# Kernel optimization log

Measured on AMD Instinct MI355X. Metric: run time of the kernel, lower is better.

Reference implementation:

```python
import jax, jax.numpy as jnp
import numpy as np

N, S, H, FA = 16, 64, 256, 256  # batch, sentences, memory_size, fact_attn_hidden


def setup_inputs() -> dict:
    key = jax.random.key(0)
    ks = jax.random.split(key, 12)
    g = lambda k, shp: (jax.random.normal(k, shp, jnp.float32) * 0.05)
    return dict(
        facts=jax.random.normal(ks[0], (N, S, H), jnp.float32),
        prevM=jax.random.normal(ks[1], (N, S, H), jnp.float32),
        questions=jax.random.normal(ks[2], (N, S, H), jnp.float32),
        doc_len=jax.random.randint(ks[3], (N,), S // 2, S + 1),
        z1_w=g(ks[4], (FA, 4 * H)), z1_b=jnp.zeros((FA,), jnp.float32),
        z2_w=g(ks[5], (1, FA)), z2_b=jnp.zeros((1,), jnp.float32),
        Wr_w=g(ks[6], (H, H)), Wr_b=jnp.zeros((H,), jnp.float32),
        Ur_w=g(ks[7], (H, H)), Ur_b=jnp.zeros((H,), jnp.float32),
        W_w=g(ks[8], (H, H)), W_b=jnp.zeros((H,), jnp.float32),
        U_w=g(ks[9], (H, H)), U_b=jnp.zeros((H,), jnp.float32),
        nm_w=g(ks[10], (H, 3 * H)), nm_b=jnp.zeros((H,), jnp.float32),
    )


def reference(facts, prevM, questions, doc_len,
              z1_w, z1_b, z2_w, z2_b,
              Wr_w, Wr_b, Ur_w, Ur_b, W_w, W_b, U_w, U_b,
              nm_w, nm_b):
    n, s, h = facts.shape
    # ---- make_interaction: pairwise features (query axis = dim1, fact/key axis = dim2)
    f = facts[:, None, :, :]       # (N,1,S,H) broadcast over queries
    m = prevM[:, :, None, :]       # (N,S,1,H) broadcast over keys
    q = questions[:, :, None, :]   # (N,S,1,H)
    z = jnp.concatenate([f * q, f * m, jnp.abs(f - q), jnp.abs(f - m)], axis=-1)  # (N,S,S,4H)
    Gh = jnp.tanh(z @ z1_w.T + z1_b)               # (N,S,S,FA)
    G = (Gh @ z2_w.T + z2_b)[..., 0]               # (N,S,S)
    mask = (jnp.arange(s) < doc_len[:, None]).astype(G.dtype)  # (N,S) key mask
    Gm = G * mask[:, None, :]
    Gm = jnp.where(Gm == 0, -jnp.inf, Gm)          # faithful to G[G==0] = -inf
    attn = jax.nn.softmax(Gm, axis=2)              # (N,S,S)

    # ---- AttentionalGRU over the S facts for each of the N*S query rows
    B = n * s
    fb = jnp.broadcast_to(facts[:, None], (n, s, s, h)).reshape(B, s, h)  # (B,S,H)
    gb = attn.reshape(B, s)                                               # (B,S)

    def step(C, xs):
        fact, gt = xs                                   # fact: (B,H), gt: (B,)
        r = jax.nn.sigmoid(fact @ Wr_w.T + Wr_b + C @ Ur_w.T + Ur_b)
        h_t = jnp.tanh(fact @ W_w.T + W_b + r * (C @ U_w.T + U_b))
        gt = gt[:, None]
        return gt * h_t + (1.0 - gt) * C, None

    C0 = jnp.zeros((B, h), facts.dtype)
    C, _ = jax.lax.scan(step, C0, (fb.transpose(1, 0, 2), gb.T))  # scan over S steps
    C = C.reshape(n, s, h)

    # ---- memory update (dropouts are identity in eval mode)
    concat = jnp.concatenate([prevM, C, questions], axis=-1)  # (N,S,3H)
    next_mem = jax.nn.relu(concat @ nm_w.T + nm_b)            # (N,S,H)
    return next_mem, attn
```

## Files before the change

### kernel.cpp

```cpp
#include <hip/hip_runtime.h>
#include <hip/hip_bf16.h>
#include <math.h>

#define NB 16
#define SS 64
#define HH 256
#define FAA 256

using short8 = __attribute__((ext_vector_type(8))) short;
using f32x4  = __attribute__((ext_vector_type(4))) float;

__device__ __forceinline__ unsigned int cvtpk(float a, float b) {
  unsigned int r;
  asm("v_cvt_pk_bf16_f32 %0, %1, %2" : "=v"(r) : "v"(a), "v"(b));
  return r;
}
__device__ __forceinline__ float sel4(const f32x4 a, int q) {
  const float s01 = (q & 1) ? a[1] : a[0];
  const float s23 = (q & 1) ? a[3] : a[2];
  return (q & 2) ? s23 : s01;
}

__global__ __launch_bounds__(256) void prolog_fused(
    const float* __restrict__ z1w, const float* __restrict__ Ur,
    const float* __restrict__ U, const float* __restrict__ nmw,
    const float* __restrict__ pm, const float* __restrict__ qs,
    unsigned short* __restrict__ z1wbf, unsigned short* __restrict__ wcatbf,
    unsigned short* __restrict__ nmbf, unsigned short* __restrict__ pmbf,
    unsigned short* __restrict__ qbf,
    const float* __restrict__ facts, const float* __restrict__ Wr,
    const float* __restrict__ Wrb, const float* __restrict__ Urb,
    const float* __restrict__ Ww, const float* __restrict__ Wb,
    float* __restrict__ FWr, float* __restrict__ FW) {
  __shared__ float fl[4][HH];
  const int bid = blockIdx.x, tid = threadIdx.x;

  auto cvt8 = [&](const float* src, unsigned short* dst, int base) {
    const float4 a = *(const float4*)(src + base);
    const float4 b = *(const float4*)(src + base + 4);
    uint4 o;
    o.x = cvtpk(a.x, a.y); o.y = cvtpk(a.z, a.w);
    o.z = cvtpk(b.x, b.y); o.w = cvtpk(b.z, b.w);
    *(uint4*)(dst + base) = o;
  };
  auto cvt8perm = [&](const float* row, unsigned short* dst, int sbase, int c0) {
    const float4 lo = *(const float4*)(row + c0);
    const float4 hi = *(const float4*)(row + c0 + 16);
    uint4 o;
    o.x = cvtpk(lo.x, hi.x); o.y = cvtpk(lo.y, hi.y);
    o.z = cvtpk(lo.z, hi.z); o.w = cvtpk(lo.w, hi.w);
    *(uint4*)(dst + sbase) = o;
  };

  if (bid < 128) {
    const int base = (bid * 256 + tid) * 8;
    cvt8(z1w, z1wbf, base);
    return;
  }
  if (bid < 192) {
    const int base = ((bid - 128) * 256 + tid) * 8;
    const int o = base >> 8, s0 = base & 255;
    const int gb = s0 & ~31, t0 = s0 & 31;
    const float* row = (o < 256) ? (Ur + o * 256) : (U + (o - 256) * 256);
    cvt8perm(row, wcatbf, base, gb + (t0 >> 1));
    return;
  }
  if (bid < 288) {
    const int base = ((bid - 192) * 256 + tid) * 8;
    const int o = base / 768, k0 = base - o * 768;
    const float* row = nmw + o * 768;
    if (k0 >= 256 && k0 < 512) {
      const int s0 = k0 - 256, gb = s0 & ~31, t0 = s0 & 31;
      cvt8perm(row, nmbf, base, 256 + gb + (t0 >> 1));
    } else {
      cvt8(row, nmbf + o * 768, k0);
    }
    return;
  }
  if (bid < 416) {
    const int base = ((bid - 288) * 256 + tid) * 8;
    cvt8(pm, pmbf, base);
    return;
  }
  if (bid < 544) {
    const int base = ((bid - 416) * 256 + tid) * 8;
    cvt8(qs, qbf, base);
    return;
  }
  const int b0 = (bid - 544) * 4;
#pragma unroll
  for (int r = 0; r < 4; ++r) fl[r][tid] = facts[(b0 + r) * HH + tid];
  __syncthreads();
  float ar[4] = {0.f, 0.f, 0.f, 0.f}, aw[4] = {0.f, 0.f, 0.f, 0.f};
  const float4* wr = (const float4*)(Wr + tid * HH);
  const float4* ww = (const float4*)(Ww + tid * HH);
  for (int d4 = 0; d4 < 64; ++d4) {
    float4 a = wr[d4], b = ww[d4];
#pragma unroll
    for (int r = 0; r < 4; ++r) {
      float4 f = *(const float4*)&fl[r][d4 * 4];
      ar[r] += a.x * f.x + a.y * f.y + a.z * f.z + a.w * f.w;
      aw[r] += b.x * f.x + b.y * f.y + b.z * f.z + b.w * f.w;
    }
  }
  const float br = Wrb[tid] + Urb[tid], bw = Wb[tid];
#pragma unroll
  for (int r = 0; r < 4; ++r) {
    FWr[(b0 + r) * HH + tid] = ar[r] + br;
    FW[(b0 + r) * HH + tid] = aw[r] + bw;
  }
}

__global__ __launch_bounds__(512, 4) void gate_gemm(
    const float* __restrict__ facts, const float* __restrict__ prevM,
    const float* __restrict__ questions, const unsigned short* __restrict__ z1wbf,
    const float* __restrict__ z1b, const float* __restrict__ z2w,
    const float* __restrict__ z2b, const int* __restrict__ doc_len,
    float* __restrict__ attn) {
  __shared__ unsigned short Ab[3][128 * 32];
  __shared__ unsigned short Bb[3][256 * 32];
  __shared__ float Gpart[128][4];

  const int bi = blockIdx.x;
  const int n = bi >> 5, i0 = (bi & 31) * 2;
  const int tid = threadIdx.x;
  const int w = tid >> 6, l = tid & 63;
  const int rg = w >> 2, cg = w & 3;
  const int l15 = l & 15, q = l >> 4;
  const int t15 = tid & 15, jb = tid >> 4;

  const float* fn = facts + n * SS * HH;
  const float* qn = questions + (n * SS + i0) * HH;
  const float* mn = prevM + (n * SS + i0) * HH;

  auto stageB = [&](int buf, int c) {
    const int kb = (c & 3) * 256 + (c >> 2) * 32;
    const int swz = ((l & 3) ^ ((l >> 2) & 3)) * 8;
#pragma unroll
    for (int j = 0; j < 2; ++j) {
      const int colg = w * 32 + j * 16 + (l >> 2);
      const unsigned short* src = z1wbf + colg * 1024 + kb + swz;
      __builtin_amdgcn_global_load_lds(src, Bb[buf] + (w * 32 + j * 16) * 32, 16, 0, 0);
    }
  };

  auto buildA = [&](int buf, int s, float2 f0, float2 f1, float2 q0, float2 q1,
                    float2 m0, float2 m1) {
    unsigned int* dst = (unsigned int*)Ab[buf];
    const int dsw = t15 ^ ((jb & 3) << 2);
    const float2 o0 = (s & 1) ? m0 : q0;
    const float2 o1 = (s & 1) ? m1 : q1;
#pragma unroll
    for (int pl = 0; pl < 2; ++pl) {
      const float fx = pl ? f1.x : f0.x;
      const float fy = pl ? f1.y : f0.y;
#pragma unroll
      for (int il = 0; il < 2; ++il) {
        const int row = il * 64 + pl * 32 + jb;
        const float ox = il ? o1.x : o0.x;
        const float oy = il ? o1.y : o0.y;
        float a, b;
        if (s < 2) { a = fx * ox;         b = fy * oy; }
        else       { a = fabsf(fx - ox);  b = fabsf(fy - oy); }
        dst[row * 16 + dsw] = cvtpk(a, b);
      }
    }
  };

  const f32x4 zero4 = {0.f, 0.f, 0.f, 0.f};
  f32x4 acc[4][4];
#pragma unroll
  for (int a = 0; a < 4; ++a)
#pragma unroll
    for (int b = 0; b < 4; ++b) acc[a][b] = zero4;

  auto mfmaStep = [&](int buf) {
    short8 Bfr[4];
#pragma unroll
    for (int nf = 0; nf < 4; ++nf) {
      const int col = cg * 64 + nf * 16 + l15;
      Bfr[nf] = *(const short8*)&Bb[buf][col * 32 + (q ^ (l15 & 3)) * 8];
    }
    __builtin_amdgcn_s_setprio(1);
#pragma unroll
    for (int mf = 0; mf < 4; ++mf) {
      const int row = rg * 64 + mf * 16 + l15;
      const short8 Afm = *(const short8*)&Ab[buf][row * 32 + (q ^ (l15 & 3)) * 8];
#pragma unroll
      for (int nf = 0; nf < 4; ++nf)
        acc[mf][nf] = __builtin_amdgcn_mfma_f32_16x16x32_bf16(Afm, Bfr[nf], acc[mf][nf], 0, 0, 0);
    }
    __builtin_amdgcn_s_setprio(0);
  };

  const int hh2 = t15 * 2;
  auto pf = [&](int hc, float2& f0, float2& f1, float2& q0, float2& q1,
                float2& m0, float2& m1) {
    const int h = hc * 32 + hh2;
    f0 = *(const float2*)(fn + jb * HH + h);
    f1 = *(const float2*)(fn + (jb + 32) * HH + h);
    q0 = *(const float2*)(qn + h);
    q1 = *(const float2*)(qn + HH + h);
    m0 = *(const float2*)(mn + h);
    m1 = *(const float2*)(mn + HH + h);
  };

  float2 Rf0, Rf1, Rq0, Rq1, Rm0, Rm1;
  float2 Sf0, Sf1, Sq0, Sq1, Sm0, Sm1;
  pf(0, Rf0, Rf1, Rq0, Rq1, Rm0, Rm1);
  stageB(0, 0);
  stageB(1, 1);
  buildA(0, 0, Rf0, Rf1, Rq0, Rq1, Rm0, Rm1);
  asm volatile("s_waitcnt vmcnt(2) lgkmcnt(0)\n\ts_barrier" ::: "memory");

#pragma unroll
  for (int c = 0; c < 32; ++c) {
    const int s = c & 3, hc = c >> 2;
    const int cb = c % 3, nb2 = (c + 1) % 3, fb = (c + 2) % 3;
    const bool pfphase = (s == 2) && (hc < 7);

    if (c + 2 < 32) stageB(fb, c + 2);
    if (pfphase) pf(hc + 1, Sf0, Sf1, Sq0, Sq1, Sm0, Sm1);
    if (c + 1 < 32) {
      if (((c + 1) & 3) == 0)
        buildA(nb2, 0, Sf0, Sf1, Sq0, Sq1, Sm0, Sm1);
      else
        buildA(nb2, (c + 1) & 3, Rf0, Rf1, Rq0, Rq1, Rm0, Rm1);
    }
    mfmaStep(cb);

    if (c <= 29) {
      if (pfphase)
        asm volatile("s_waitcnt vmcnt(8) lgkmcnt(0)\n\ts_barrier" ::: "memory");
      else
        asm volatile("s_waitcnt vmcnt(2) lgkmcnt(0)\n\ts_barrier" ::: "memory");
    } else if (c == 30) {
      asm volatile("s_waitcnt vmcnt(0) lgkmcnt(0)\n\ts_barrier" ::: "memory");
    }
    if (s == 3) {
      Rf0 = Sf0; Rf1 = Sf1; Rq0 = Sq0; Rq1 = Sq1; Rm0 = Sm0; Rm1 = Sm1;
    }
  }

  float psum[4][4];
#pragma unroll
  for (int mf = 0; mf < 4; ++mf)
#pragma unroll
    for (int v = 0; v < 4; ++v) psum[mf][v] = 0.f;

#pragma unroll
  for (int nf = 0; nf < 4; ++nf) {
    const int k = cg * 64 + nf * 16 + l15;
    const float zb = z1b[k], zw = z2w[k];
#pragma unroll
    for (int mf = 0; mf < 4; ++mf)
#pragma unroll
      for (int v = 0; v < 4; ++v) {
        const float x = acc[mf][nf][v] + zb;
        const float e = __expf(2.f * x);
        const float t = 1.f - 2.f / (e + 1.f);
        psum[mf][v] += zw * t;
      }
  }
#pragma unroll
  for (int d = 1; d < 16; d <<= 1)
#pragma unroll
    for (int mf = 0; mf < 4; ++mf)
#pragma unroll
      for (int v = 0; v < 4; ++v) psum[mf][v] += __shfl_xor(psum[mf][v], d, 64);
  if (l15 == 0) {
#pragma unroll
    for (int mf = 0; mf < 4; ++mf)
#pragma unroll
      for (int v = 0; v < 4; ++v)
        Gpart[rg * 64 + mf * 16 + q * 4 + v][cg] = psum[mf][v];
  }
  __syncthreads();
  if (tid < 128) {
    const float gg = Gpart[tid][0] + Gpart[tid][1] + Gpart[tid][2] + Gpart[tid][3] + z2b[0];
    const int i = i0 + (tid >> 6), j = tid & 63;
    const int dl = doc_len[n];
    const float x = (j < dl && gg != 0.0f) ? gg : -INFINITY;
    float mx = x;
#pragma unroll
    for (int d = 1; d < 64; d <<= 1) mx = fmaxf(mx, __shfl_xor(mx, d, 64));
    const float e = (x == -INFINITY) ? 0.f : __expf(x - mx);
    float s = e;
#pragma unroll
    for (int d = 1; d < 64; d <<= 1) s += __shfl_xor(s, d, 64);
    attn[(n * SS + i) * SS + j] = e / s;
  }
}

__global__ __launch_bounds__(512, 2) void gru_scan(
    const unsigned short* __restrict__ wcat, const float* __restrict__ FWr,
    const float* __restrict__ FW, const float* __restrict__ Ub,
    const float* __restrict__ attn, unsigned short* __restrict__ Cout,
    float* __restrict__ cm0save, float* __restrict__ cm1save, const int part) {
  __shared__ unsigned short Cbf[2][4 * 272];
  __shared__ float attn_sT[64 * 4];

  const int bi = blockIdx.x, n = bi >> 4, i0 = (bi & 15) * 4;
  const int tid = threadIdx.x, w = tid >> 6, l = tid & 63;
  const int l15 = l & 15, q = l >> 4;
  const int h0 = w * 32 + l15;

  short8 Bf[8][4];
#pragma unroll
  for (int f = 0; f < 4; ++f) {
    const int wrow = ((f >> 1) ? 256 : 0) + w * 32 + (f & 1) * 16 + l15;
    const unsigned short* bb = wcat + wrow * 256 + q * 8;
#pragma unroll
    for (int kt = 0; kt < 8; ++kt)
      Bf[kt][f] = *(const short8*)(bb + kt * 32);
  }

  const float ub0 = Ub[h0], ub1 = Ub[h0 + 16];

  for (int e = tid; e < 64 * 4; e += 512)
    attn_sT[e] = attn[(n * SS + i0 + (e & 3)) * SS + (e >> 2)];

  float cm0, cm1;
  if (part == 0) {
    for (int e = tid; e < 544; e += 512)
      ((unsigned int*)Cbf[0])[e] = 0u;
    cm0 = 0.f; cm1 = 0.f;
  } else {
    cm0 = cm0save[bi * 512 + tid];
    cm1 = cm1save[bi * 512 + tid];
    ((unsigned int*)Cbf[0])[q * 136 + w * 16 + l15] = cvtpk(cm0, cm1);
  }
  __syncthreads();

  const float* fwr_g = FWr + n * SS * HH;
  const float* fw_g  = FW + n * SS * HH;

  const int tbeg = part ? 32 : 0, tend = part ? 64 : 32;
  float fr0 = fwr_g[tbeg * HH + h0], fr1 = fwr_g[tbeg * HH + h0 + 16];
  float fc0 = fw_g[tbeg * HH + h0],  fc1 = fw_g[tbeg * HH + h0 + 16];

  for (int t = tbeg; t < tend; ++t) {
    const int cur = t & 1;
    const unsigned short* Cr = Cbf[cur];
    unsigned int* Cw = (unsigned int*)Cbf[cur ^ 1];

    short8 Af[8];
    const int arow = (l15 & 3) * 272;
#pragma unroll
    for (int kt = 0; kt < 8; ++kt)
      Af[kt] = *(const short8*)&Cr[arow + kt * 32 + q * 8];

    float nr0 = 0.f, nr1 = 0.f, nc0 = 0.f, nc1 = 0.f;
    if (t < 63) {
      nr0 = fwr_g[(t + 1) * HH + h0];
      nr1 = fwr_g[(t + 1) * HH + h0 + 16];
      nc0 = fw_g[(t + 1) * HH + h0];
      nc1 = fw_g[(t + 1) * HH + h0 + 16];
    }

    const f32x4 z4 = {0.f, 0.f, 0.f, 0.f};
    f32x4 a0 = z4, a1 = z4, a2 = z4, a3 = z4;
    __builtin_amdgcn_s_setprio(1);
#pragma unroll
    for (int kt = 0; kt < 8; ++kt) {
      a0 = __builtin_amdgcn_mfma_f32_16x16x32_bf16(Af[kt], Bf[kt][0], a0, 0, 0, 0);
      a2 = __builtin_amdgcn_mfma_f32_16x16x32_bf16(Af[kt], Bf[kt][2], a2, 0, 0, 0);
    }
#pragma unroll
    for (int kt = 0; kt < 8; ++kt) {
      a1 = __builtin_amdgcn_mfma_f32_16x16x32_bf16(Af[kt], Bf[kt][1], a1, 0, 0, 0);
      a3 = __builtin_amdgcn_mfma_f32_16x16x32_bf16(Af[kt], Bf[kt][3], a3, 0, 0, 0);
    }
    __builtin_amdgcn_s_setprio(0);

    const float g = attn_sT[t * 4 + q];

    const float yr0 = sel4(a0, q), yu0 = sel4(a2, q);
    const float r0 = 1.f / (1.f + __expf(-(fr0 + yr0)));
    const float x0 = fc0 + r0 * (yu0 + ub0);
    const float e0 = __expf(2.f * x0);
    const float h0t = 1.f - 2.f / (e0 + 1.f);
    cm0 += g * (h0t - cm0);

    const float yr1 = sel4(a1, q), yu1 = sel4(a3, q);
    const float r1 = 1.f / (1.f + __expf(-(fr1 + yr1)));
    const float x1 = fc1 + r1 * (yu1 + ub1);
    const float e1 = __expf(2.f * x1);
    const float h1t = 1.f - 2.f / (e1 + 1.f);
    cm1 += g * (h1t - cm1);

    Cw[q * 136 + w * 16 + l15] = cvtpk(cm0, cm1);

    fr0 = nr0; fr1 = nr1; fc0 = nc0; fc1 = nc1;
    __syncthreads();
  }

  if (part == 0) {
    cm0save[bi * 512 + tid] = cm0;
    cm1save[bi * 512 + tid] = cm1;
    return;
  }
  {
    const int row = tid >> 7, wo = tid & 127;
    ((unsigned int*)Cout)[(n * SS + i0 + row) * 128 + wo] =
        *(const unsigned int*)&Cbf[0][row * 272 + wo * 2];
  }
}

__global__ __launch_bounds__(128) void next_mem_gemm(
    const unsigned short* __restrict__ pmbf, const unsigned short* __restrict__ cbf,
    const unsigned short* __restrict__ qbf, const unsigned short* __restrict__ nmbf,
    const float* __restrict__ nmb, float* __restrict__ out) {
  const int bi = blockIdx.x;
  const int rb = bi >> 3, cb = bi & 7;
  const int r0 = rb * 32, c0 = cb * 32;
  const int tid = threadIdx.x, w = tid >> 6, l = tid & 63;
  const int l15 = l & 15, q = l >> 4;

  const int arow = (r0 + w * 16 + l15) * HH + q * 8;
  const unsigned short* nb = nmbf + (c0 + l15) * 768 + q * 8;

  const f32x4 z4 = {0.f, 0.f, 0.f, 0.f};
  f32x4 acc0 = z4, acc1 = z4;

#pragma unroll
  for (int kt = 0; kt < 8; ++kt) {
    const short8 Af = *(const short8*)(pmbf + arow + kt * 32);
    const short8 B0 = *(const short8*)(nb + kt * 32);
    const short8 B1 = *(const short8*)(nb + 16 * 768 + kt * 32);
    acc0 = __builtin_amdgcn_mfma_f32_16x16x32_bf16(Af, B0, acc0, 0, 0, 0);
    acc1 = __builtin_amdgcn_mfma_f32_16x16x32_bf16(Af, B1, acc1, 0, 0, 0);
  }
#pragma unroll
  for (int kt = 0; kt < 8; ++kt) {
    const short8 Af = *(const short8*)(cbf + arow + kt * 32);
    const short8 B0 = *(const short8*)(nb + 256 + kt * 32);
    const short8 B1 = *(const short8*)(nb + 16 * 768 + 256 + kt * 32);
    acc0 = __builtin_amdgcn_mfma_f32_16x16x32_bf16(Af, B0, acc0, 0, 0, 0);
    acc1 = __builtin_amdgcn_mfma_f32_16x16x32_bf16(Af, B1, acc1, 0, 0, 0);
  }
#pragma unroll
  for (int kt = 0; kt < 8; ++kt) {
    const short8 Af = *(const short8*)(qbf + arow + kt * 32);
    const short8 B0 = *(const short8*)(nb + 512 + kt * 32);
    const short8 B1 = *(const short8*)(nb + 16 * 768 + 512 + kt * 32);
    acc0 = __builtin_amdgcn_mfma_f32_16x16x32_bf16(Af, B0, acc0, 0, 0, 0);
    acc1 = __builtin_amdgcn_mfma_f32_16x16x32_bf16(Af, B1, acc1, 0, 0, 0);
  }

#pragma unroll
  for (int nf = 0; nf < 2; ++nf) {
    const int col = c0 + nf * 16 + l15;
    const float bv = nmb[col];
    const f32x4 a = nf ? acc1 : acc0;
#pragma unroll
    for (int v = 0; v < 4; ++v) {
      const int grow = r0 + w * 16 + q * 4 + v;
      out[grow * HH + col] = fmaxf(a[v] + bv, 0.f);
    }
  }
}

extern "C" void kernel_launch(void* const* d_in, const int* in_sizes, int n_in,
                              void* d_out, int out_size, void* d_ws, size_t ws_size,
                              hipStream_t stream) {
  const float* facts     = (const float*)d_in[0];
  const float* prevM     = (const float*)d_in[1];
  const float* questions = (const float*)d_in[2];
  const int*   doc_len   = (const int*)d_in[3];
  const float* z1w = (const float*)d_in[4];
  const float* z1b = (const float*)d_in[5];
  const float* z2w = (const float*)d_in[6];
  const float* z2b = (const float*)d_in[7];
  const float* Wrw = (const float*)d_in[8];
  const float* Wrb = (const float*)d_in[9];
  const float* Urw = (const float*)d_in[10];
  const float* Urb = (const float*)d_in[11];
  const float* Ww  = (const float*)d_in[12];
  const float* Wb  = (const float*)d_in[13];
  const float* Uw  = (const float*)d_in[14];
  const float* Ub  = (const float*)d_in[15];
  const float* nmw = (const float*)d_in[16];
  const float* nmb = (const float*)d_in[17];

  char* ws = (char*)d_ws;
  unsigned short* z1wbf  = (unsigned short*)(ws + 0);
  unsigned short* wcatbf = (unsigned short*)(ws + 524288);
  unsigned short* nmbf   = (unsigned short*)(ws + 786432);
  unsigned short* pmbf   = (unsigned short*)(ws + 1179648);
  unsigned short* qbf    = (unsigned short*)(ws + 1703936);
  float* FWr = (float*)(ws + 2490368);
  float* FW  = (float*)(ws + 3538944);
  unsigned short* cbf = (unsigned short*)(ws + 4587520);

  float* cm0save = (float*)(ws + 0);
  float* cm1save = (float*)(ws + 4587520);

  float* out  = (float*)d_out;
  float* attn = out + NB * SS * HH;

  prolog_fused<<<800, 256, 0, stream>>>(z1w, Urw, Uw, nmw, prevM, questions,
                                        z1wbf, wcatbf, nmbf, pmbf, qbf,
                                        facts, Wrw, Wrb, Urb, Ww, Wb, FWr, FW);
  gate_gemm<<<512, 512, 0, stream>>>(facts, prevM, questions, z1wbf, z1b, z2w, z2b,
                                     doc_len, attn);
  gru_scan<<<256, 512, 0, stream>>>(wcatbf, FWr, FW, Ub, attn, cbf, cm0save, cm1save, 0);
  gru_scan<<<256, 512, 0, stream>>>(wcatbf, FWr, FW, Ub, attn, cbf, cm0save, cm1save, 1);
  next_mem_gemm<<<256, 128, 0, stream>>>(pmbf, cbf, qbf, nmbf, nmb, out);
}
```

Baseline: 241.1 us.

## Drop register double-buffering of interaction operands and reorder MFMA-first loop

Removes the second register set (S*) that prefetched the next chunk's facts, question and memory values a step early. The next chunk is now loaded into the live registers right before the A tile is built. The loop now runs the MFMA step first, then the loads and A-tile build, and the full unroll pragma is dropped. The aim is lower register pressure and simpler wait counts. In exchange, global-load latency is exposed once every four iterations, and the loop may lose static unrolling.

New measurement: 237.7 us. Within noise of the previous version (-1.4%).

```diff
diff --git a/kernel.cpp b/kernel.cpp
--- a/kernel.cpp
+++ b/kernel.cpp
@@ -194,51 +194,38 @@
   };
 
   const int hh2 = t15 * 2;
-  auto pf = [&](int hc, float2& f0, float2& f1, float2& q0, float2& q1,
-                float2& m0, float2& m1) {
+  float2 Rf0, Rf1, Rq0, Rq1, Rm0, Rm1;
+  auto pf = [&](int hc) {
     const int h = hc * 32 + hh2;
-    f0 = *(const float2*)(fn + jb * HH + h);
-    f1 = *(const float2*)(fn + (jb + 32) * HH + h);
-    q0 = *(const float2*)(qn + h);
-    q1 = *(const float2*)(qn + HH + h);
-    m0 = *(const float2*)(mn + h);
-    m1 = *(const float2*)(mn + HH + h);
-  };
-
-  float2 Rf0, Rf1, Rq0, Rq1, Rm0, Rm1;
-  float2 Sf0, Sf1, Sq0, Sq1, Sm0, Sm1;
-  pf(0, Rf0, Rf1, Rq0, Rq1, Rm0, Rm1);
+    Rf0 = *(const float2*)(fn + jb * HH + h);
+    Rf1 = *(const float2*)(fn + (jb + 32) * HH + h);
+    Rq0 = *(const float2*)(qn + h);
+    Rq1 = *(const float2*)(qn + HH + h);
+    Rm0 = *(const float2*)(mn + h);
+    Rm1 = *(const float2*)(mn + HH + h);
+  };
+
+  pf(0);
   stageB(0, 0);
   stageB(1, 1);
   buildA(0, 0, Rf0, Rf1, Rq0, Rq1, Rm0, Rm1);
   asm volatile("s_waitcnt vmcnt(2) lgkmcnt(0)\n\ts_barrier" ::: "memory");
 
-#pragma unroll
   for (int c = 0; c < 32; ++c) {
     const int s = c & 3, hc = c >> 2;
     const int cb = c % 3, nb2 = (c + 1) % 3, fb = (c + 2) % 3;
-    const bool pfphase = (s == 2) && (hc < 7);
-
+
+    mfmaStep(cb);
+
+    if (s == 3 && hc < 7) pf(hc + 1);
     if (c + 2 < 32) stageB(fb, c + 2);
-    if (pfphase) pf(hc + 1, Sf0, Sf1, Sq0, Sq1, Sm0, Sm1);
-    if (c + 1 < 32) {
-      if (((c + 1) & 3) == 0)
-        buildA(nb2, 0, Sf0, Sf1, Sq0, Sq1, Sm0, Sm1);
-      else
-        buildA(nb2, (c + 1) & 3, Rf0, Rf1, Rq0, Rq1, Rm0, Rm1);
-    }
-    mfmaStep(cb);
+    if (c + 1 < 32)
+      buildA(nb2, (c + 1) & 3, Rf0, Rf1, Rq0, Rq1, Rm0, Rm1);
 
     if (c <= 29) {
-      if (pfphase)
-        asm volatile("s_waitcnt vmcnt(8) lgkmcnt(0)\n\ts_barrier" ::: "memory");
-      else
-        asm volatile("s_waitcnt vmcnt(2) lgkmcnt(0)\n\ts_barrier" ::: "memory");
+      asm volatile("s_waitcnt vmcnt(2) lgkmcnt(0)\n\ts_barrier" ::: "memory");
     } else if (c == 30) {
       asm volatile("s_waitcnt vmcnt(0) lgkmcnt(0)\n\ts_barrier" ::: "memory");
-    }
-    if (s == 3) {
-      Rf0 = Sf0; Rf1 = Sf1; Rq0 = Sq0; Rq1 = Sq1; Rm0 = Sm0; Rm1 = Sm1;
     }
   }
 
```
